# Performance work log

Measured on AMD Instinct MI355X. Metric: run time of the kernel, lower is better.

Reference implementation:

```python
import jax, jax.numpy as jnp
import numpy as np

KH = KW = 3
K = KH * KW
OG = 1  # offset_groups
WG = 1  # weight_groups
DIL = 1

def _conv_same(x, w):
    # stride-1 SAME NCHW conv, matching the keras offset/mask convs
    return jax.lax.conv_general_dilated(
        x, w, window_strides=(1, 1), padding='SAME',
        dimension_numbers=('NCHW', 'OIHW', 'NCHW'))

def _deform_conv2d(x, w, offset, mask):
    # x: [B,C,H,W]; w: [F, C//WG, KH, KW]
    # offset: [B, OG*2*K, H, W] laid out as (og, k, {dy,dx});
    # mask:   [B, OG*K, H, W]
    B, C, H, W = x.shape
    F = w.shape[0]
    pad_h = ((KH - 1) * DIL) // 2
    pad_w = ((KW - 1) * DIL) // 2
    ky = jnp.arange(KH) * DIL - pad_h
    kx = jnp.arange(KW) * DIL - pad_w
    kyy, kxx = jnp.meshgrid(ky, kx, indexing='ij')
    kyy = kyy.reshape(K).astype(x.dtype)
    kxx = kxx.reshape(K).astype(x.dtype)

    off = offset.reshape(B, OG, K, 2, H, W)
    dy = off[:, :, :, 0]  # [B,OG,K,H,W]
    dx = off[:, :, :, 1]
    oy = jnp.arange(H, dtype=x.dtype)
    ox = jnp.arange(W, dtype=x.dtype)
    y = oy[None, None, None, :, None] + kyy[None, None, :, None, None] + dy
    xq = ox[None, None, None, None, :] + kxx[None, None, :, None, None] + dx

    y0 = jnp.floor(y)
    x0 = jnp.floor(xq)
    wy = y - y0   # [B,OG,K,H,W]
    wx = xq - x0
    y0i = y0.astype(jnp.int32)
    x0i = x0.astype(jnp.int32)

    Cg = C // OG
    xg = x.reshape(B, OG, Cg, H * W)

    def gather(yi, xi):
        valid = (yi >= 0) & (yi < H) & (xi >= 0) & (xi < W)
        idx = jnp.clip(yi, 0, H - 1) * W + jnp.clip(xi, 0, W - 1)
        flat = idx.reshape(B, OG, 1, K * H * W)
        v = jnp.take_along_axis(xg, flat, axis=3)   # [B,OG,Cg,K*H*W]
        v = v.reshape(B, OG, Cg, K, H, W)
        return v * valid[:, :, None].astype(x.dtype)

    v00 = gather(y0i, x0i)
    v01 = gather(y0i, x0i + 1)
    v10 = gather(y0i + 1, x0i)
    v11 = gather(y0i + 1, x0i + 1)
    wy_ = wy[:, :, None]
    wx_ = wx[:, :, None]
    samp = (v00 * (1 - wy_) * (1 - wx_) + v01 * (1 - wy_) * wx_
            + v10 * wy_ * (1 - wx_) + v11 * wy_ * wx_)  # [B,OG,Cg,K,H,W]
    m = mask.reshape(B, OG, K, H, W)[:, :, None]
    samp = samp * m
    wr = w.reshape(F, OG, Cg, K)
    return jnp.einsum('bgckhw,fgck->bfhw', samp, wr)


def setup_inputs() -> dict:
    key = jax.random.key(0)
    k1, k2, k3, k4 = jax.random.split(key, 4)
    B, C, H, W = 8, 256, 64, 64
    F = 256
    x = jax.random.normal(k1, (B, C, H, W), dtype=jnp.float32)
    w_offset = jax.random.normal(k2, (OG * 2 * K, C, KH, KW), dtype=jnp.float32) * 0.01
    w_mask = jax.random.normal(k3, (OG * K, C, KH, KW), dtype=jnp.float32) * 0.01
    w_deform = jax.random.normal(k4, (F, C // WG, KH, KW), dtype=jnp.float32) * 0.05
    return {'x': x, 'w_offset': w_offset, 'w_mask': w_mask, 'w_deform': w_deform}


def reference(x, w_offset, w_mask, w_deform):
    offset = _conv_same(x, w_offset)                 # [B, 2K, H, W]
    mask = jax.nn.sigmoid(_conv_same(x, w_mask))     # [B, K, H, W]
    return _deform_conv2d(x, w_deform, offset, mask)
```

## Files before the change

kernel.cpp:

```cpp
#include <hip/hip_runtime.h>
#include <hip/hip_bf16.h>
#include <hip/hip_fp16.h>
#include <math.h>

constexpr int Bn = 8, Cn = 256, Hn = 64, Wn = 64, Fn = 256, Kn = 9;
constexpr int HWn = Hn * Wn;
constexpr int NM = Bn * Kn * HWn;
constexpr int NCH = 4;

using frag_ab = __attribute__((ext_vector_type(8))) short;
using frag_h  = __attribute__((ext_vector_type(8))) _Float16;
using f32x4   = __attribute__((ext_vector_type(4))) float;

__device__ inline ushort f2bf(float f) {
    union { float f; uint32_t u; } un{f};
    return (ushort)((un.u + 0x7FFF + ((un.u >> 16) & 1)) >> 16);
}
__device__ inline ushort f2h(float f) {
    __half h = __float2half_rn(f);
    return *reinterpret_cast<ushort*>(&h);
}

__global__ __launch_bounds__(256) void wtrans2(const float* __restrict__ wd,
                                               ushort* __restrict__ wB) {
    int i = blockIdx.x * 256 + threadIdx.x;
    if (i >= Fn * Cn * Kn) return;
    int ci = i & 7, fi = (i >> 3) & 15, G = (i >> 7) & 31, ft = (i >> 12) & 15, k = i >> 16;
    int f = ft * 16 + fi, c = G * 8 + ci;
    wB[i] = f2h(wd[(f * Cn + c) * 9 + k]);
}

__global__ __launch_bounds__(256) void wpack27(const float* __restrict__ wo,
                                               const float* __restrict__ wm,
                                               ushort* __restrict__ wA) {
    int i = blockIdx.x * 256 + threadIdx.x;
    if (i >= 73728) return;
    int ci = i & 7, l = (i >> 3) & 63, mt = (i >> 9) & 1, cblk = (i >> 10) & 7, tap = i >> 13;
    int m = mt * 16 + (l & 15);
    int c = cblk * 32 + ((l >> 4) & 3) * 8 + ci;
    float v = 0.f;
    if (m < 18)      v = wo[(m * Cn + c) * 9 + tap];
    else if (m < 27) v = wm[((m - 18) * Cn + c) * 9 + tap];
    wA[i] = f2bf(v);
}

__global__ __launch_bounds__(256) void xpose(const float* __restrict__ x,
                                             __half2* __restrict__ xh) {
    int i = blockIdx.x * 256 + threadIdx.x;
    int p = i & 4095, q = (i >> 12) & 3, b = i >> 14;
    const float* xp = x + (size_t)b * Cn * HWn + p;
    __half2* op = xh + (((size_t)b * 4096 + p) << 7) + q * 32;
#pragma unroll
    for (int j = 0; j < 32; ++j) {
        int c = q * 64 + 2 * j;
        op[j] = __float22half2_rn(make_float2(xp[(size_t)c * HWn],
                                              xp[(size_t)(c + 1) * HWn]));
    }
}

__global__ __launch_bounds__(256) void offconv27(const float* __restrict__ x,
                                                 const ushort* __restrict__ wA,
                                                 float* __restrict__ part) {
    __shared__ ushort xs[4][66][40];
    const int t = threadIdx.x;
    const int l = t & 63, w = t >> 6;
    const int li = l & 15, lg = l >> 4;
    const int rb = blockIdx.x, ch = blockIdx.y, b = blockIdx.z;
    const int h0 = rb * 2;
    const int rw = w >> 1, pt0 = (w & 1) * 2;

    f32x4 acc[2][2];
#pragma unroll
    for (int mt = 0; mt < 2; ++mt)
#pragma unroll
        for (int q = 0; q < 2; ++q) acc[mt][q] = (f32x4)0.f;

    const float* xb = x + (size_t)b * Cn * HWn;

#pragma unroll 1
    for (int cc = 0; cc < 2; ++cc) {
        const int cbase = ch * 64 + cc * 32;
        __syncthreads();
        for (int j = t; j < 1056; j += 256) {
            int cq = j / 264;
            int rem = j - cq * 264;
            int r = rem / 66, col = rem - r * 66;
            int rg = h0 - 1 + r, cg = col - 1;
            ushort u[8];
            if ((unsigned)rg < (unsigned)Hn && (unsigned)cg < (unsigned)Wn) {
                const float* xp = xb + (size_t)(cbase + cq * 8) * HWn + (rg << 6) + cg;
#pragma unroll
                for (int jj = 0; jj < 8; ++jj) u[jj] = f2bf(xp[(size_t)jj * HWn]);
            } else {
#pragma unroll
                for (int jj = 0; jj < 8; ++jj) u[jj] = 0;
            }
            *(int4*)&xs[r][col][cq * 8] =
                make_int4(u[0] | (u[1] << 16), u[2] | (u[3] << 16),
                          u[4] | (u[5] << 16), u[6] | (u[7] << 16));
        }
        __syncthreads();
        const int cblk = ch * 2 + cc;
#pragma unroll
        for (int tap = 0; tap < 9; ++tap) {
            const int ky = tap / 3, kx = tap - 3 * (tap / 3);
            frag_ab a0 = *(const frag_ab*)(wA + (size_t)((tap * 8 + cblk) * 2) * 512 + l * 8);
            frag_ab a1 = *(const frag_ab*)(wA + (size_t)((tap * 8 + cblk) * 2 + 1) * 512 + l * 8);
#pragma unroll
            for (int q = 0; q < 2; ++q) {
                frag_ab bf = *(const frag_ab*)&xs[rw + ky][(pt0 + q) * 16 + li + kx][lg * 8];
                acc[0][q] = __builtin_amdgcn_mfma_f32_16x16x32_bf16(a0, bf, acc[0][q], 0, 0, 0);
                acc[1][q] = __builtin_amdgcn_mfma_f32_16x16x32_bf16(a1, bf, acc[1][q], 0, 0, 0);
            }
        }
    }

    const int h = h0 + rw;
#pragma unroll
    for (int mt = 0; mt < 2; ++mt)
#pragma unroll
        for (int j = 0; j < 4; ++j) {
            int m = mt * 16 + lg * 4 + j;
            if (m < 27) {
#pragma unroll
                for (int q = 0; q < 2; ++q) {
                    int pixel = (pt0 + q) * 16 + li;
                    part[((size_t)((ch * Bn + b) * 27 + m) << 12) + (h << 6) + pixel] =
                        acc[mt][q][j];
                }
            }
        }
}

__global__ __launch_bounds__(256) void metafin9(const float* __restrict__ part,
                                                int4* __restrict__ mpack) {
    const int k = blockIdx.y;
    const int idx = blockIdx.x * 256 + threadIdx.x;
    const int b = idx >> 12, p = idx & 4095;
    const int h = p >> 6, w = p & 63;

    float dy = 0.f, dx = 0.f, ms = 0.f;
#pragma unroll
    for (int ch = 0; ch < NCH; ++ch) {
        size_t base = ((size_t)((ch * Bn + b) * 27) << 12) + p;
        dy += part[base + ((size_t)(2 * k) << 12)];
        dx += part[base + ((size_t)(2 * k + 1) << 12)];
        ms += part[base + ((size_t)(18 + k) << 12)];
    }
    float m = 1.f / (1.f + expf(-ms));
    float yy = (float)(h + k / 3 - 1) + dy;
    float xx = (float)(w + k % 3 - 1) + dx;
    float y0f = floorf(yy), x0f = floorf(xx);
    float wy = yy - y0f, wx = xx - x0f;
    int y0 = (int)y0f, x0 = (int)x0f;
    int y1 = y0 + 1, x1 = x0 + 1;
    bool vy0 = (unsigned)y0 < (unsigned)Hn;
    bool vx0 = (unsigned)x0 < (unsigned)Wn;
    bool vy1 = (unsigned)y1 < (unsigned)Hn;
    bool vx1 = (unsigned)x1 < (unsigned)Wn;
    int cy0 = min(max(y0, 0), Hn - 1), cx0 = min(max(x0, 0), Wn - 1);
    int cy1 = min(max(y1, 0), Hn - 1), cx1 = min(max(x1, 0), Wn - 1);
    float w00 = (vy0 && vx0) ? (1.f - wy) * (1.f - wx) * m : 0.f;
    float w01 = (vy0 && vx1) ? (1.f - wy) * wx * m : 0.f;
    float w10 = (vy1 && vx0) ? wy * (1.f - wx) * m : 0.f;
    float w11 = (vy1 && vx1) ? wy * wx * m : 0.f;
    int i00 = (cy0 << 6) + cx0, i01 = (cy0 << 6) + cx1;
    int i10 = (cy1 << 6) + cx0, i11 = (cy1 << 6) + cx1;
    union { struct { __half a, bh; } h; int i; } pz, pw;
    pz.h.a = __float2half_rn(w00); pz.h.bh = __float2half_rn(w01);
    pw.h.a = __float2half_rn(w10); pw.h.bh = __float2half_rn(w11);
    int q = ((b * 9 + k) << 12) + p;
    mpack[q] = make_int4(i00 | (i01 << 16), i10 | (i11 << 16), pz.i, pw.i);
}

__global__ __launch_bounds__(512, 4) void dconv(const uint32_t* __restrict__ xh,
                                                const ushort* __restrict__ wB,
                                                const int4* __restrict__ mpack,
                                                float* __restrict__ out) {
    __shared__ uint32_t sl[2][64][20];
    __shared__ int4 ml[9][64];
    const int t = threadIdx.x;
    const int l = t & 63, w = t >> 6;
    const int li = l & 15, lg = l >> 4;
    const int pu = (w << 3) + (l >> 3);
    const int g  = l & 7;
    const int b = blockIdx.x;
    const int p0 = blockIdx.y << 6;

    f32x4 acc[2][4];
#pragma unroll
    for (int a = 0; a < 2; ++a)
#pragma unroll
        for (int q = 0; q < 4; ++q) acc[a][q] = (f32x4)0.f;

    const uint32_t* xb = xh + ((size_t)b << 19);

    for (int j = t; j < 576; j += 512)
        ml[j >> 6][j & 63] = mpack[((b * 9 + (j >> 6)) << 12) + p0 + (j & 63)];
    __syncthreads();

    auto STAGE = [&](int s, int buf) {
        const int k = s % 9, ch = s / 9;
        const int4 m = ml[k][pu];
        const int i00 = m.x & 0xFFFF, i01 = ((unsigned)m.x) >> 16;
        const int i10 = m.y & 0xFFFF, i11 = ((unsigned)m.y) >> 16;
        union { int i; __half2 h; } uz, uw;
        uz.i = m.z; uw.i = m.w;
        const uint32_t* base = xb + (ch << 4) + (g << 1);
        uint2 v00 = *(const uint2*)(base + i00 * 128);
        uint2 v01 = *(const uint2*)(base + i01 * 128);
        uint2 v10 = *(const uint2*)(base + i10 * 128);
        uint2 v11 = *(const uint2*)(base + i11 * 128);
        const __half2 w00 = __half2half2(__low2half(uz.h));
        const __half2 w01 = __half2half2(__high2half(uz.h));
        const __half2 w10 = __half2half2(__low2half(uw.h));
        const __half2 w11 = __half2half2(__high2half(uw.h));
        __half2 r0 = __hmul2(w00, *(__half2*)&v00.x);
        r0 = __hfma2(w01, *(__half2*)&v01.x, r0);
        r0 = __hfma2(w10, *(__half2*)&v10.x, r0);
        r0 = __hfma2(w11, *(__half2*)&v11.x, r0);
        __half2 r1 = __hmul2(w00, *(__half2*)&v00.y);
        r1 = __hfma2(w01, *(__half2*)&v01.y, r1);
        r1 = __hfma2(w10, *(__half2*)&v10.y, r1);
        r1 = __hfma2(w11, *(__half2*)&v11.y, r1);
        uint2 rr;
        rr.x = *(uint32_t*)&r0;
        rr.y = *(uint32_t*)&r1;
        *(uint2*)&sl[buf][pu][g << 1] = rr;
    };

    auto COMPUTE = [&](int s, int buf) {
        const int k = s % 9, ch = s / 9;
        frag_h bq[4];
#pragma unroll
        for (int pt = 0; pt < 4; ++pt)
            bq[pt] = *(const frag_h*)&sl[buf][pt * 16 + li][lg << 2];
#pragma unroll
        for (int ft = 0; ft < 2; ++ft) {
            frag_h a = *(const frag_h*)(wB + (((size_t)(k * 16 + 2 * w + ft)) << 12)
                                           + (ch << 9) + (l << 3));
#pragma unroll
            for (int pt = 0; pt < 4; ++pt)
                acc[ft][pt] = __builtin_amdgcn_mfma_f32_16x16x32_f16(
                    a, bq[pt], acc[ft][pt], 0, 0, 0);
        }
    };

    STAGE(0, 0);
    __syncthreads();
#pragma unroll 1
    for (int s = 0; s < 72; ++s) {
        const int cur = s & 1;
        if (s + 1 < 72) STAGE(s + 1, cur ^ 1);
        COMPUTE(s, cur);
        __syncthreads();
    }

    float* ob = out + (size_t)b * Fn * HWn + p0;
#pragma unroll
    for (int ft = 0; ft < 2; ++ft)
#pragma unroll
        for (int j = 0; j < 4; ++j) {
            int f = w * 32 + ft * 16 + lg * 4 + j;
#pragma unroll
            for (int pt = 0; pt < 4; ++pt)
                ob[(size_t)f * HWn + pt * 16 + li] = acc[ft][pt][j];
        }
}

extern "C" void kernel_launch(void* const* d_in, const int* in_sizes, int n_in,
                              void* d_out, int out_size, void* d_ws, size_t ws_size,
                              hipStream_t stream) {
    const float* x  = (const float*)d_in[0];
    const float* wo = (const float*)d_in[1];
    const float* wm = (const float*)d_in[2];
    const float* wd = (const float*)d_in[3];
    float* out = (float*)d_out;

    int4*     mpack = (int4*)d_ws;
    char*     region = (char*)d_ws + (size_t)NM * 16;
    float*    part  = (float*)region;
    ushort*   wBp   = (ushort*)region;
    __half2*  xhh   = (__half2*)(region + 1179648);
    uint32_t* xhu   = (uint32_t*)(region + 1179648);
    ushort*   wA27  = (ushort*)(region + 18874368);

    wpack27<<<dim3(288), dim3(256), 0, stream>>>(wo, wm, wA27);
    offconv27<<<dim3(32, NCH, Bn), dim3(256), 0, stream>>>(x, wA27, part);
    metafin9<<<dim3(Bn * HWn / 256, 9), dim3(256), 0, stream>>>(part, mpack);
    wtrans2<<<dim3((Fn * Cn * Kn + 255) / 256), dim3(256), 0, stream>>>(wd, wBp);
    xpose<<<dim3(Bn * 4 * HWn / 256), dim3(256), 0, stream>>>(x, xhh);
    dconv<<<dim3(Bn, HWn / 64), dim3(512), 0, stream>>>(xhu, wBp, mpack, out);
}
```

Baseline: 118.7 us.

## Double channel chunk per pipeline stage with 16-byte gathers and XOR-swizzled LDS

```diff
diff --git a/kernel.cpp b/kernel.cpp
--- a/kernel.cpp
+++ b/kernel.cpp
@@ -177,7 +177,7 @@
                                                 const ushort* __restrict__ wB,
                                                 const int4* __restrict__ mpack,
                                                 float* __restrict__ out) {
-    __shared__ uint32_t sl[2][64][20];
+    __shared__ ushort sl[2][64][64];
     __shared__ int4 ml[9][64];
     const int t = threadIdx.x;
     const int l = t & 63, w = t >> 6;
@@ -206,52 +206,74 @@
         const int i10 = m.y & 0xFFFF, i11 = ((unsigned)m.y) >> 16;
         union { int i; __half2 h; } uz, uw;
         uz.i = m.z; uw.i = m.w;
-        const uint32_t* base = xb + (ch << 4) + (g << 1);
-        uint2 v00 = *(const uint2*)(base + i00 * 128);
-        uint2 v01 = *(const uint2*)(base + i01 * 128);
-        uint2 v10 = *(const uint2*)(base + i10 * 128);
-        uint2 v11 = *(const uint2*)(base + i11 * 128);
+        const uint32_t* base = xb + (ch << 5) + (g << 2);
+        uint4 v00 = *(const uint4*)(base + (size_t)i00 * 128);
+        uint4 v01 = *(const uint4*)(base + (size_t)i01 * 128);
+        uint4 v10 = *(const uint4*)(base + (size_t)i10 * 128);
+        uint4 v11 = *(const uint4*)(base + (size_t)i11 * 128);
         const __half2 w00 = __half2half2(__low2half(uz.h));
         const __half2 w01 = __half2half2(__high2half(uz.h));
         const __half2 w10 = __half2half2(__low2half(uw.h));
         const __half2 w11 = __half2half2(__high2half(uw.h));
-        __half2 r0 = __hmul2(w00, *(__half2*)&v00.x);
-        r0 = __hfma2(w01, *(__half2*)&v01.x, r0);
-        r0 = __hfma2(w10, *(__half2*)&v10.x, r0);
-        r0 = __hfma2(w11, *(__half2*)&v11.x, r0);
-        __half2 r1 = __hmul2(w00, *(__half2*)&v00.y);
-        r1 = __hfma2(w01, *(__half2*)&v01.y, r1);
-        r1 = __hfma2(w10, *(__half2*)&v10.y, r1);
-        r1 = __hfma2(w11, *(__half2*)&v11.y, r1);
-        uint2 rr;
-        rr.x = *(uint32_t*)&r0;
-        rr.y = *(uint32_t*)&r1;
-        *(uint2*)&sl[buf][pu][g << 1] = rr;
+        uint4 rr;
+        {
+            __half2 r = __hmul2(w00, *(__half2*)&v00.x);
+            r = __hfma2(w01, *(__half2*)&v01.x, r);
+            r = __hfma2(w10, *(__half2*)&v10.x, r);
+            r = __hfma2(w11, *(__half2*)&v11.x, r);
+            rr.x = *(uint32_t*)&r;
+        }
+        {
+            __half2 r = __hmul2(w00, *(__half2*)&v00.y);
+            r = __hfma2(w01, *(__half2*)&v01.y, r);
+            r = __hfma2(w10, *(__half2*)&v10.y, r);
+            r = __hfma2(w11, *(__half2*)&v11.y, r);
+            rr.y = *(uint32_t*)&r;
+        }
+        {
+            __half2 r = __hmul2(w00, *(__half2*)&v00.z);
+            r = __hfma2(w01, *(__half2*)&v01.z, r);
+            r = __hfma2(w10, *(__half2*)&v10.z, r);
+            r = __hfma2(w11, *(__half2*)&v11.z, r);
+            rr.z = *(uint32_t*)&r;
+        }
+        {
+            __half2 r = __hmul2(w00, *(__half2*)&v00.w);
+            r = __hfma2(w01, *(__half2*)&v01.w, r);
+            r = __hfma2(w10, *(__half2*)&v10.w, r);
+            r = __hfma2(w11, *(__half2*)&v11.w, r);
+            rr.w = *(uint32_t*)&r;
+        }
+        *(uint4*)&sl[buf][pu][(g ^ (pu & 7)) << 3] = rr;
     };
 
     auto COMPUTE = [&](int s, int buf) {
         const int k = s % 9, ch = s / 9;
-        frag_h bq[4];
-#pragma unroll
-        for (int pt = 0; pt < 4; ++pt)
-            bq[pt] = *(const frag_h*)&sl[buf][pt * 16 + li][lg << 2];
-#pragma unroll
-        for (int ft = 0; ft < 2; ++ft) {
-            frag_h a = *(const frag_h*)(wB + (((size_t)(k * 16 + 2 * w + ft)) << 12)
-                                           + (ch << 9) + (l << 3));
+        const ushort* wp = wB + ((size_t)((k * 16 + 2 * w) * 512 + ch * 128)) * 8;
+#pragma unroll
+        for (int h = 0; h < 2; ++h) {
+            frag_h bq[4];
 #pragma unroll
             for (int pt = 0; pt < 4; ++pt)
-                acc[ft][pt] = __builtin_amdgcn_mfma_f32_16x16x32_f16(
-                    a, bq[pt], acc[ft][pt], 0, 0, 0);
+                bq[pt] = *(const frag_h*)&sl[buf][pt * 16 + li]
+                                           [((((h << 2) | lg) ^ (l & 7)) << 3)];
+#pragma unroll
+            for (int ft = 0; ft < 2; ++ft) {
+                frag_h a = *(const frag_h*)(wp + (size_t)(ft * 512 + h * 64 + l) * 8);
+#pragma unroll
+                for (int pt = 0; pt < 4; ++pt)
+                    acc[ft][pt] = __builtin_amdgcn_mfma_f32_16x16x32_f16(
+                        a, bq[pt], acc[ft][pt], 0, 0, 0);
+            }
         }
     };
 
     STAGE(0, 0);
     __syncthreads();
 #pragma unroll 1
-    for (int s = 0; s < 72; ++s) {
+    for (int s = 0; s < 36; ++s) {
         const int cur = s & 1;
-        if (s + 1 < 72) STAGE(s + 1, cur ^ 1);
+        if (s + 1 < 36) STAGE(s + 1, cur ^ 1);
         COMPUTE(s, cur);
         __syncthreads();
     }
```

Measured after the change: 106.1 us. 1.12x faster.
